# Optimization experiments

Hardware: AMD Instinct MI355X
Metric: run time of the kernel (lower is better)

## Reference

```python
import jax, jax.numpy as jnp
import numpy as np

NUM_HEADS = 16

def setup_inputs() -> dict:
    key = jax.random.key(0)
    ks = jax.random.split(key, 7)
    query_dim, kv_dim, out_dim = 1024, 768, 1024
    N, Lq, Lkv = 4, 2048, 2048
    s_q = 1.0 / np.sqrt(query_dim)
    s_kv = 1.0 / np.sqrt(kv_dim)
    return {
        "query": jax.random.normal(ks[0], (N, Lq, query_dim), dtype=jnp.float32),
        "kv": jax.random.normal(ks[1], (N, Lkv, kv_dim), dtype=jnp.float32),
        # Linear weights stored as (in_dim, out_dim) for x @ W
        "Wq": jax.random.uniform(ks[2], (query_dim, query_dim), jnp.float32, -s_q, s_q),
        "Wk": jax.random.uniform(ks[3], (kv_dim, query_dim), jnp.float32, -s_kv, s_kv),
        "Wv": jax.random.uniform(ks[4], (kv_dim, query_dim), jnp.float32, -s_kv, s_kv),
        "Wo": jax.random.uniform(ks[5], (query_dim, out_dim), jnp.float32, -s_q, s_q),
        "bo": jax.random.uniform(ks[6], (out_dim,), jnp.float32, -s_q, s_q),
    }

def reference(query, kv, Wq, Wk, Wv, Wo, bo):
    N, Lq, qd = query.shape
    Lkv = kv.shape[1]
    H = NUM_HEADS
    hd = qd // H
    scale = hd ** -0.5
    # projections -> (N, H, L, hd)
    q = (query @ Wq).reshape(N, Lq, H, hd).transpose(0, 2, 1, 3)
    k = (kv @ Wk).reshape(N, Lkv, H, hd).transpose(0, 2, 1, 3)
    v = (kv @ Wv).reshape(N, Lkv, H, hd).transpose(0, 2, 1, 3)
    # fp32 attention: (N, H, Lq, Lkv)
    attn = jnp.einsum('bhqd,bhkd->bhqk', q.astype(jnp.float32) * scale, k.astype(jnp.float32))
    attn = jax.nn.softmax(attn, axis=-1)
    out = jnp.einsum('bhqk,bhkd->bhqd', attn, v.astype(jnp.float32))
    out = out.transpose(0, 2, 1, 3).reshape(N, Lq, qd)
    return out @ Wo + bo
```

## Files before the change

kernel.cpp:

```cpp
#include <hip/hip_runtime.h>

typedef __attribute__((ext_vector_type(4))) float f32x4;
typedef __attribute__((ext_vector_type(8))) __bf16 bf16x8;
typedef __attribute__((ext_vector_type(8))) unsigned short us8;

__device__ __forceinline__ unsigned short f2bf(float f) {
    unsigned u = __builtin_bit_cast(unsigned, f);
    u += 0x7fffu + ((u >> 16) & 1u);
    return (unsigned short)(u >> 16);
}

__device__ __forceinline__ float exp2v(float x) {
    float r;
    asm("v_exp_f32 %0, %1" : "=v"(r) : "v"(x));
    return r;
}

__device__ __forceinline__ f32x4 mfma16(bf16x8 a, bf16x8 b, f32x4 c) {
    return __builtin_amdgcn_mfma_f32_16x16x32_bf16(a, b, c, 0, 0, 0);
}

__device__ __forceinline__ void gload16(const void* g, void* l) {
    __builtin_amdgcn_global_load_lds(
        (const __attribute__((address_space(1))) unsigned int*)g,
        (__attribute__((address_space(3))) unsigned int*)l, 16, 0, 0);
}

__global__ __launch_bounds__(256) void conv2_bf16(const float* __restrict__ a,
                                                  unsigned short* __restrict__ oa,
                                                  int na8,
                                                  const float* __restrict__ b,
                                                  unsigned short* __restrict__ ob,
                                                  int nb8) {
    int i = blockIdx.x * 256 + threadIdx.x;
    const float* in;
    unsigned short* out;
    if (i < na8) {
        in = a; out = oa;
    } else {
        i -= na8;
        if (i >= nb8) return;
        in = b; out = ob;
    }
    const float4* p = (const float4*)in + (size_t)i * 2;
    float4 x = p[0], y = p[1];
    us8 o;
    o[0] = f2bf(x.x); o[1] = f2bf(x.y); o[2] = f2bf(x.z); o[3] = f2bf(x.w);
    o[4] = f2bf(y.x); o[5] = f2bf(y.y); o[6] = f2bf(y.z); o[7] = f2bf(y.w);
    *((us8*)out + i) = o;
}

__global__ __launch_bounds__(256) void wtrans_all(const float* __restrict__ Wq,
                                                  const float* __restrict__ Wk,
                                                  const float* __restrict__ Wv,
                                                  const float* __restrict__ Wo,
                                                  unsigned short* __restrict__ WqT,
                                                  unsigned short* __restrict__ WkT,
                                                  unsigned short* __restrict__ WvT,
                                                  unsigned short* __restrict__ WoT,
                                                  float qscale) {
    __shared__ float t[32][33];
    int y = blockIdx.y;
    const float* in; unsigned short* out; int R; float scale = 1.0f;
    if (y < 32)      { in = Wq; out = WqT; R = 1024; scale = qscale; }
    else if (y < 56) { in = Wk; out = WkT; R = 768;  y -= 32; }
    else if (y < 80) { in = Wv; out = WvT; R = 768;  y -= 56; }
    else             { in = Wo; out = WoT; R = 1024; y -= 80; }
    int tx = threadIdx.x, ty = threadIdx.y;
    int r0 = y * 32, c0 = blockIdx.x * 32;
#pragma unroll
    for (int k = 0; k < 4; ++k)
        t[ty + k * 8][tx] = in[(size_t)(r0 + ty + k * 8) * 1024 + c0 + tx];
    __syncthreads();
#pragma unroll
    for (int k = 0; k < 4; ++k)
        out[(size_t)(c0 + ty + k * 8) * R + r0 + tx] = f2bf(t[tx][ty + k * 8] * scale);
}

template <int KD, int EPI>
__global__ __launch_bounds__(256, 4) void gemm_bf16(const unsigned short* __restrict__ A,
                                                    const unsigned short* __restrict__ B,
                                                    void* __restrict__ Cout,
                                                    const float* __restrict__ bias) {
    __shared__ __align__(16) unsigned short SL[2][8192];
    const int m0 = blockIdx.y * 128;
    const int n0 = blockIdx.x * 128;
    const int tid = threadIdx.x;
    const int w = tid >> 6, l = tid & 63;
    const int lr = l & 15, lg = l >> 4;
    const int wm = (w >> 1) * 64, wn = (w & 1) * 64;

    f32x4 acc[4][4] = {};

    int ci0 = w * 64 + l;
    int r0 = ci0 >> 2, c0 = (ci0 & 3) ^ (r0 & 3);
    int ci1 = 256 + ci0;
    int r1 = ci1 >> 2, c1 = (ci1 & 3) ^ (r1 & 3);

    const unsigned short* Ag0 = A + (size_t)(m0 + r0) * KD + c0 * 8;
    const unsigned short* Ag1 = A + (size_t)(m0 + r1) * KD + c1 * 8;
    const unsigned short* Bg0 = B + (size_t)(n0 + r0) * KD + c0 * 8;
    const unsigned short* Bg1 = B + (size_t)(n0 + r1) * KD + c1 * 8;

#define STG(buf, k0)                                                  \
    do {                                                              \
        gload16(Ag0 + (k0), &SL[buf][w * 512]);                       \
        gload16(Ag1 + (k0), &SL[buf][2048 + w * 512]);                \
        gload16(Bg0 + (k0), &SL[buf][4096 + w * 512]);                \
        gload16(Bg1 + (k0), &SL[buf][4096 + 2048 + w * 512]);         \
    } while (0)

    constexpr int NT = KD / 32;
    STG(0, 0);
    int buf = 0;
    for (int kt = 0; kt < NT; ++kt) {
        if (kt + 1 < NT) {
            STG(buf ^ 1, (kt + 1) * 32);
            asm volatile("s_waitcnt vmcnt(4)" ::: "memory");
        } else {
            asm volatile("s_waitcnt vmcnt(0)" ::: "memory");
        }
        __builtin_amdgcn_s_barrier();
        const unsigned short* Alc = &SL[buf][0];
        const unsigned short* Blc = &SL[buf][4096];
        bf16x8 af[4], bfr[4];
#pragma unroll
        for (int t = 0; t < 4; ++t) {
            int ar = wm + t * 16 + lr;
            af[t] = *(const bf16x8*)&Alc[ar * 32 + ((lg ^ (ar & 3)) * 8)];
            int br = wn + t * 16 + lr;
            bfr[t] = *(const bf16x8*)&Blc[br * 32 + ((lg ^ (br & 3)) * 8)];
        }
#pragma unroll
        for (int i = 0; i < 4; ++i)
#pragma unroll
            for (int j = 0; j < 4; ++j)
                acc[i][j] = mfma16(af[i], bfr[j], acc[i][j]);
        __builtin_amdgcn_s_barrier();
        buf ^= 1;
    }
#undef STG

#pragma unroll
    for (int i = 0; i < 4; ++i)
#pragma unroll
        for (int j = 0; j < 4; ++j)
#pragma unroll
            for (int r = 0; r < 4; ++r) {
                int m = m0 + wm + i * 16 + lg * 4 + r;
                int n = n0 + wn + j * 16 + lr;
                if (EPI == 0) {
                    int b = m >> 11, ql = m & 2047, h = n >> 6, d = n & 63;
                    ((unsigned short*)Cout)[(((size_t)(b * 16 + h) * 2048 + ql) << 6) + d] =
                        f2bf(acc[i][j][r]);
                } else {
                    ((float*)Cout)[(size_t)m * 1024 + n] = acc[i][j][r] + bias[n];
                }
            }
}

__global__ __launch_bounds__(256, 4) void gemm_kv(const unsigned short* __restrict__ A,
                                                  const unsigned short* __restrict__ Bk,
                                                  const unsigned short* __restrict__ Bv,
                                                  unsigned short* __restrict__ Ck,
                                                  unsigned short* __restrict__ Cv) {
    constexpr int KD = 768;
    __shared__ __align__(16) unsigned short SL[2][8192];
    const int isV = blockIdx.x >> 3;
    const int n0 = (blockIdx.x & 7) * 128;
    const int m0 = blockIdx.y * 128;
    const unsigned short* B = isV ? Bv : Bk;
    const int tid = threadIdx.x;
    const int w = tid >> 6, l = tid & 63;
    const int lr = l & 15, lg = l >> 4;
    const int wm = (w >> 1) * 64, wn = (w & 1) * 64;

    f32x4 acc[4][4] = {};

    int ci0 = w * 64 + l;
    int r0 = ci0 >> 2, c0 = (ci0 & 3) ^ (r0 & 3);
    int ci1 = 256 + ci0;
    int r1 = ci1 >> 2, c1 = (ci1 & 3) ^ (r1 & 3);

    const unsigned short* Ag0 = A + (size_t)(m0 + r0) * KD + c0 * 8;
    const unsigned short* Ag1 = A + (size_t)(m0 + r1) * KD + c1 * 8;
    const unsigned short* Bg0 = B + (size_t)(n0 + r0) * KD + c0 * 8;
    const unsigned short* Bg1 = B + (size_t)(n0 + r1) * KD + c1 * 8;

#define STG(buf, k0)                                                  \
    do {                                                              \
        gload16(Ag0 + (k0), &SL[buf][w * 512]);                       \
        gload16(Ag1 + (k0), &SL[buf][2048 + w * 512]);                \
        gload16(Bg0 + (k0), &SL[buf][4096 + w * 512]);                \
        gload16(Bg1 + (k0), &SL[buf][4096 + 2048 + w * 512]);         \
    } while (0)

    constexpr int NT = KD / 32;
    STG(0, 0);
    int buf = 0;
    for (int kt = 0; kt < NT; ++kt) {
        if (kt + 1 < NT) {
            STG(buf ^ 1, (kt + 1) * 32);
            asm volatile("s_waitcnt vmcnt(4)" ::: "memory");
        } else {
            asm volatile("s_waitcnt vmcnt(0)" ::: "memory");
        }
        __builtin_amdgcn_s_barrier();
        const unsigned short* Alc = &SL[buf][0];
        const unsigned short* Blc = &SL[buf][4096];
        bf16x8 af[4], bfr[4];
#pragma unroll
        for (int t = 0; t < 4; ++t) {
            int ar = wm + t * 16 + lr;
            af[t] = *(const bf16x8*)&Alc[ar * 32 + ((lg ^ (ar & 3)) * 8)];
            int br = wn + t * 16 + lr;
            bfr[t] = *(const bf16x8*)&Blc[br * 32 + ((lg ^ (br & 3)) * 8)];
        }
#pragma unroll
        for (int i = 0; i < 4; ++i)
#pragma unroll
            for (int j = 0; j < 4; ++j)
                acc[i][j] = mfma16(af[i], bfr[j], acc[i][j]);
        __builtin_amdgcn_s_barrier();
        buf ^= 1;
    }
#undef STG

    if (!isV) {
#pragma unroll
        for (int i = 0; i < 4; ++i)
#pragma unroll
            for (int j = 0; j < 4; ++j)
#pragma unroll
                for (int r = 0; r < 4; ++r) {
                    int m = m0 + wm + i * 16 + lg * 4 + r;
                    int n = n0 + wn + j * 16 + lr;
                    int b = m >> 11, ql = m & 2047, h = n >> 6, d = n & 63;
                    Ck[(((size_t)(b * 16 + h) * 2048 + ql) << 6) + d] = f2bf(acc[i][j][r]);
                }
    } else {
        const int b = m0 >> 11;
        const int mloc = m0 & 2047;
        const int h0 = n0 >> 6;
#pragma unroll
        for (int hp = 0; hp < 2; ++hp) {
            unsigned short* VTb = Cv + (size_t)(b * 16 + h0 + hp) * (64 * 2048);
#pragma unroll
            for (int dh = 0; dh < 2; ++dh) {
                __syncthreads();
                if ((w & 1) == hp) {
#pragma unroll
                    for (int jj = 0; jj < 2; ++jj) {
                        int j = dh * 2 + jj;
                        int dl = jj * 16 + lr;
#pragma unroll
                        for (int i = 0; i < 4; ++i)
#pragma unroll
                            for (int r = 0; r < 4; ++r) {
                                int kvl = wm + i * 16 + lg * 4 + r;
                                int pl = (kvl & 0x60) | (((kvl >> 2) & 3) << 3) |
                                         (((kvl >> 4) & 1) << 2) | (kvl & 3);
                                SL[0][dl * 136 + pl] = f2bf(acc[i][j][r]);
                            }
                    }
                }
                __syncthreads();
#pragma unroll
                for (int cc = 0; cc < 2; ++cc) {
                    int idx = cc * 256 + tid;
                    int row = idx >> 4, col = (idx & 15) * 8;
                    *(us8*)&VTb[(size_t)(dh * 32 + row) * 2048 + mloc + col] =
                        *(const us8*)&SL[0][row * 136 + col];
                }
            }
        }
    }
}

__global__ __launch_bounds__(256, 4) void attn_fwd(const unsigned short* __restrict__ Q,
                                                   const unsigned short* __restrict__ K,
                                                   const unsigned short* __restrict__ VT,
                                                   unsigned short* __restrict__ O) {
    __shared__ __align__(16) unsigned short Kl[2][64 * 64];
    __shared__ __align__(16) unsigned short Vl[2][64 * 64];
    const int id = blockIdx.x;
    const int sw = (id & 7) * 128 + (id >> 3);
    const int qt = sw & 15, bh = sw >> 4;
    const int tid = threadIdx.x;
    const int w = tid >> 6, l = tid & 63;
    const int lr = l & 15, lg = l >> 4;
    const size_t hbase = (size_t)bh * (2048 * 64);
    const size_t vbase = (size_t)bh * (64 * 2048);
    const int qbase = qt * 128 + w * 32;

    bf16x8 qf[2][2];
#pragma unroll
    for (int rt = 0; rt < 2; ++rt) {
        const unsigned short* qp = Q + hbase + (size_t)(qbase + rt * 16 + lr) * 64;
        qf[rt][0] = *(const bf16x8*)(qp + lg * 8);
        qf[rt][1] = *(const bf16x8*)(qp + 32 + lg * 8);
    }

    f32x4 oacc[2][4] = {};
    f32x4 lacc[2] = {};
    const f32x4 FZERO = {};

    bf16x8 ONES;
#pragma unroll
    for (int e = 0; e < 8; ++e) ONES[e] = (__bf16)1.0f;

    const int cA = tid, cB = 256 + tid;
    const int krA = cA >> 3, kcA = (cA & 7) ^ (krA & 7);
    const int krB = cB >> 3, kcB = (cB & 7) ^ (krB & 7);
    const unsigned short* Kg0 = K + hbase + (size_t)krA * 64 + kcA * 8;
    const unsigned short* Kg1 = K + hbase + (size_t)krB * 64 + kcB * 8;
    const unsigned short* Vg0 = VT + vbase + (size_t)krA * 2048 + kcA * 8;
    const unsigned short* Vg1 = VT + vbase + (size_t)krB * 2048 + kcB * 8;

#define STAGE_KV(dst, kv0)                                                    \
    do {                                                                      \
        gload16(Kg0 + (size_t)(kv0) * 64, &Kl[dst][w * 512]);                 \
        gload16(Kg1 + (size_t)(kv0) * 64, &Kl[dst][2048 + w * 512]);          \
        gload16(Vg0 + (kv0), &Vl[dst][w * 512]);                              \
        gload16(Vg1 + (kv0), &Vl[dst][2048 + w * 512]);                       \
    } while (0)

    const int koff0 = lr * 64 + ((lg ^ (lr & 7)) * 8);
    const int koff1 = lr * 64 + (((4 + lg) ^ (lr & 7)) * 8);

    STAGE_KV(0, 0);
    int cur = 0;

    for (int t = 0; t < 32; ++t) {
        if (t < 31) {
            STAGE_KV(cur ^ 1, (t + 1) * 64);
            asm volatile("s_waitcnt vmcnt(4)" ::: "memory");
        } else {
            asm volatile("s_waitcnt vmcnt(0)" ::: "memory");
        }
        __builtin_amdgcn_s_barrier();
        const unsigned short* Kc = Kl[cur];
        const unsigned short* Vc = Vl[cur];

        f32x4 s[2][4];
        __builtin_amdgcn_s_setprio(1);
#pragma unroll
        for (int nt = 0; nt < 4; ++nt) {
            bf16x8 kf0 = *(const bf16x8*)&Kc[koff0 + nt * 1024];
            bf16x8 kf1 = *(const bf16x8*)&Kc[koff1 + nt * 1024];
            s[0][nt] = mfma16(kf0, qf[0][0], FZERO);
            s[0][nt] = mfma16(kf1, qf[0][1], s[0][nt]);
            s[1][nt] = mfma16(kf0, qf[1][0], FZERO);
            s[1][nt] = mfma16(kf1, qf[1][1], s[1][nt]);
        }
        __builtin_amdgcn_s_setprio(0);

        bf16x8 pa0[2], pa1[2];
#pragma unroll
        for (int rt = 0; rt < 2; ++rt) {
#pragma unroll
            for (int nt = 0; nt < 4; ++nt)
#pragma unroll
                for (int r = 0; r < 4; ++r)
                    s[rt][nt][r] = exp2v(s[rt][nt][r]);
#pragma unroll
            for (int e = 0; e < 4; ++e) {
                pa0[rt][e] = (__bf16)s[rt][0][e];
                pa0[rt][4 + e] = (__bf16)s[rt][1][e];
                pa1[rt][e] = (__bf16)s[rt][2][e];
                pa1[rt][4 + e] = (__bf16)s[rt][3][e];
            }
        }

        __builtin_amdgcn_s_setprio(1);
        lacc[0] = mfma16(pa0[0], ONES, lacc[0]);
        lacc[0] = mfma16(pa1[0], ONES, lacc[0]);
        lacc[1] = mfma16(pa0[1], ONES, lacc[1]);
        lacc[1] = mfma16(pa1[1], ONES, lacc[1]);

#pragma unroll
        for (int nt = 0; nt < 4; ++nt) {
            bf16x8 vb0 = *(const bf16x8*)&Vc[koff0 + nt * 1024];
            bf16x8 vb1 = *(const bf16x8*)&Vc[koff1 + nt * 1024];
            oacc[0][nt] = mfma16(pa0[0], vb0, oacc[0][nt]);
            oacc[0][nt] = mfma16(pa1[0], vb1, oacc[0][nt]);
            oacc[1][nt] = mfma16(pa0[1], vb0, oacc[1][nt]);
            oacc[1][nt] = mfma16(pa1[1], vb1, oacc[1][nt]);
        }
        __builtin_amdgcn_s_setprio(0);
        __builtin_amdgcn_s_barrier();
        cur ^= 1;
    }
#undef STAGE_KV

    const int b = bh >> 4, h = bh & 15;
#pragma unroll
    for (int rt = 0; rt < 2; ++rt)
#pragma unroll
        for (int r = 0; r < 4; ++r) {
            float inv = 1.0f / lacc[rt][r];
            int q = qbase + rt * 16 + lg * 4 + r;
            size_t rowbase = ((size_t)(b * 2048 + q)) * 1024 + h * 64;
#pragma unroll
            for (int nt = 0; nt < 4; ++nt)
                O[rowbase + nt * 16 + lr] = f2bf(oacc[rt][nt][r] * inv);
        }
}

extern "C" void kernel_launch(void* const* d_in, const int* in_sizes, int n_in,
                              void* d_out, int out_size, void* d_ws, size_t ws_size,
                              hipStream_t stream) {
    (void)in_sizes; (void)n_in; (void)out_size; (void)ws_size;
    const float* query = (const float*)d_in[0];
    const float* kv    = (const float*)d_in[1];
    const float* Wq    = (const float*)d_in[2];
    const float* Wk    = (const float*)d_in[3];
    const float* Wv    = (const float*)d_in[4];
    const float* Wo    = (const float*)d_in[5];
    const float* bo    = (const float*)d_in[6];
    float* out = (float*)d_out;

    char* ws = (char*)d_ws;
    unsigned short* qbf  = (unsigned short*)(ws + 0);
    unsigned short* kvbf = (unsigned short*)(ws + 16777216);
    unsigned short* WkT  = (unsigned short*)(ws + 29360128);
    unsigned short* WvT  = (unsigned short*)(ws + 30932992);
    unsigned short* WqT  = (unsigned short*)(ws + 32505856);
    unsigned short* WoT  = (unsigned short*)(ws + 34603008);
    unsigned short* Qh   = (unsigned short*)(ws + 36700160);
    unsigned short* Kh   = (unsigned short*)(ws + 53477376);
    unsigned short* VTh  = (unsigned short*)(ws + 0);
    unsigned short* Ob   = (unsigned short*)(ws + 16777216);

    const float QSCALE = 0.18033688011112042f;

    conv2_bf16<<<7168, 256, 0, stream>>>(query, qbf, 1048576, kv, kvbf, 786432);
    wtrans_all<<<dim3(32, 112), dim3(32, 8), 0, stream>>>(Wq, Wk, Wv, Wo,
                                                          WqT, WkT, WvT, WoT, QSCALE);

    gemm_bf16<1024, 0><<<dim3(8, 64), 256, 0, stream>>>(qbf, WqT, Qh, nullptr);
    gemm_kv<<<dim3(16, 64), 256, 0, stream>>>(kvbf, WkT, WvT, Kh, VTh);
    attn_fwd<<<1024, 256, 0, stream>>>(Qh, Kh, VTh, Ob);
    gemm_bf16<1024, 1><<<dim3(8, 64), 256, 0, stream>>>(Ob, WoT, out, bo);
}
```

Measured before the change: 175.4 us.

## Merge Q/K/V projections into one launch and software-pipeline attention QK with PV

The separate Q and KV projection GEMMs become a single 1536-block launch that picks its operand by block index, with an XCD-aware block swizzle for L2 locality. The output GEMM gets the same swizzle. The attention loop is restructured so K and V tiles are staged separately and the QK^T of the next tile is issued alongside the PV of the current tile, overlapping exp work with MFMA. Attention launch bounds drop to 3 waves per SIMD to allow more registers. VTh moves to its own workspace region so it no longer aliases qbf. The cost is extra register pressure and a more complex prologue and epilogue.

```diff
diff --git a/kernel.cpp b/kernel.cpp
--- a/kernel.cpp
+++ b/kernel.cpp
@@ -77,14 +77,27 @@
         out[(size_t)(c0 + ty + k * 8) * R + r0 + tx] = f2bf(t[tx][ty + k * 8] * scale);
 }
 
-template <int KD, int EPI>
-__global__ __launch_bounds__(256, 4) void gemm_bf16(const unsigned short* __restrict__ A,
-                                                    const unsigned short* __restrict__ B,
-                                                    void* __restrict__ Cout,
-                                                    const float* __restrict__ bias) {
+__global__ __launch_bounds__(256, 4) void proj_qkv(const unsigned short* __restrict__ qbf,
+                                                   const unsigned short* __restrict__ kvbf,
+                                                   const unsigned short* __restrict__ WqT,
+                                                   const unsigned short* __restrict__ WkT,
+                                                   const unsigned short* __restrict__ WvT,
+                                                   unsigned short* __restrict__ Qh,
+                                                   unsigned short* __restrict__ Kh,
+                                                   unsigned short* __restrict__ VTh) {
     __shared__ __align__(16) unsigned short SL[2][8192];
-    const int m0 = blockIdx.y * 128;
-    const int n0 = blockIdx.x * 128;
+    const int id = blockIdx.x;
+    const int xcd = id & 7, j = id >> 3;
+    const int my = xcd * 8 + (j & 7);
+    const int rest = j >> 3;
+    const int op = rest >> 3;
+    const int nx = rest & 7;
+    const int m0 = my * 128, n0 = nx * 128;
+    const unsigned short* A = (op == 0) ? qbf : kvbf;
+    const unsigned short* B = (op == 0) ? WqT : (op == 1 ? WkT : WvT);
+    const int KD = (op == 0) ? 1024 : 768;
+    const int NT = KD >> 5;
+
     const int tid = threadIdx.x;
     const int w = tid >> 6, l = tid & 63;
     const int lr = l & 15, lg = l >> 4;
@@ -110,7 +123,6 @@
         gload16(Bg1 + (k0), &SL[buf][4096 + 2048 + w * 512]);         \
     } while (0)
 
-    constexpr int NT = KD / 32;
     STG(0, 0);
     int buf = 0;
     for (int kt = 0; kt < NT; ++kt) {
@@ -134,42 +146,75 @@
 #pragma unroll
         for (int i = 0; i < 4; ++i)
 #pragma unroll
-            for (int j = 0; j < 4; ++j)
-                acc[i][j] = mfma16(af[i], bfr[j], acc[i][j]);
+            for (int jj = 0; jj < 4; ++jj)
+                acc[i][jj] = mfma16(af[i], bfr[jj], acc[i][jj]);
         __builtin_amdgcn_s_barrier();
         buf ^= 1;
     }
 #undef STG
 
-#pragma unroll
-    for (int i = 0; i < 4; ++i)
-#pragma unroll
-        for (int j = 0; j < 4; ++j)
-#pragma unroll
-            for (int r = 0; r < 4; ++r) {
-                int m = m0 + wm + i * 16 + lg * 4 + r;
-                int n = n0 + wn + j * 16 + lr;
-                if (EPI == 0) {
+    if (op != 2) {
+        unsigned short* Cout = (op == 0) ? Qh : Kh;
+#pragma unroll
+        for (int i = 0; i < 4; ++i)
+#pragma unroll
+            for (int jj = 0; jj < 4; ++jj)
+#pragma unroll
+                for (int r = 0; r < 4; ++r) {
+                    int m = m0 + wm + i * 16 + lg * 4 + r;
+                    int n = n0 + wn + jj * 16 + lr;
                     int b = m >> 11, ql = m & 2047, h = n >> 6, d = n & 63;
-                    ((unsigned short*)Cout)[(((size_t)(b * 16 + h) * 2048 + ql) << 6) + d] =
-                        f2bf(acc[i][j][r]);
-                } else {
-                    ((float*)Cout)[(size_t)m * 1024 + n] = acc[i][j][r] + bias[n];
+                    Cout[(((size_t)(b * 16 + h) * 2048 + ql) << 6) + d] = f2bf(acc[i][jj][r]);
+                }
+    } else {
+        const int b = m0 >> 11;
+        const int mloc = m0 & 2047;
+        const int h0 = n0 >> 6;
+#pragma unroll
+        for (int hp = 0; hp < 2; ++hp) {
+            unsigned short* VTb = VTh + (size_t)(b * 16 + h0 + hp) * (64 * 2048);
+#pragma unroll
+            for (int dh = 0; dh < 2; ++dh) {
+                __syncthreads();
+                if ((w & 1) == hp) {
+#pragma unroll
+                    for (int jj = 0; jj < 2; ++jj) {
+                        int jc = dh * 2 + jj;
+                        int dl = jj * 16 + lr;
+#pragma unroll
+                        for (int i = 0; i < 4; ++i)
+#pragma unroll
+                            for (int r = 0; r < 4; ++r) {
+                                int kvl = wm + i * 16 + lg * 4 + r;
+                                int pl = (kvl & 0x60) | (((kvl >> 2) & 3) << 3) |
+                                         (((kvl >> 4) & 1) << 2) | (kvl & 3);
+                                SL[0][dl * 136 + pl] = f2bf(acc[i][jc][r]);
+                            }
+                    }
+                }
+                __syncthreads();
+#pragma unroll
+                for (int cc = 0; cc < 2; ++cc) {
+                    int idx = cc * 256 + tid;
+                    int row = idx >> 4, col = (idx & 15) * 8;
+                    *(us8*)&VTb[(size_t)(dh * 32 + row) * 2048 + mloc + col] =
+                        *(const us8*)&SL[0][row * 136 + col];
                 }
             }
-}
-
-__global__ __launch_bounds__(256, 4) void gemm_kv(const unsigned short* __restrict__ A,
-                                                  const unsigned short* __restrict__ Bk,
-                                                  const unsigned short* __restrict__ Bv,
-                                                  unsigned short* __restrict__ Ck,
-                                                  unsigned short* __restrict__ Cv) {
-    constexpr int KD = 768;
+        }
+    }
+}
+
+__global__ __launch_bounds__(256, 4) void gemm_o(const unsigned short* __restrict__ A,
+                                                 const unsigned short* __restrict__ B,
+                                                 float* __restrict__ Cout,
+                                                 const float* __restrict__ bias) {
+    constexpr int KD = 1024;
     __shared__ __align__(16) unsigned short SL[2][8192];
-    const int isV = blockIdx.x >> 3;
-    const int n0 = (blockIdx.x & 7) * 128;
-    const int m0 = blockIdx.y * 128;
-    const unsigned short* B = isV ? Bv : Bk;
+    const int id = blockIdx.x;
+    const int xcd = id & 7, j = id >> 3;
+    const int m0 = (xcd * 8 + (j & 7)) * 128;
+    const int n0 = (j >> 3) * 128;
     const int tid = threadIdx.x;
     const int w = tid >> 6, l = tid & 63;
     const int lr = l & 15, lg = l >> 4;
@@ -195,7 +240,7 @@
         gload16(Bg1 + (k0), &SL[buf][4096 + 2048 + w * 512]);         \
     } while (0)
 
-    constexpr int NT = KD / 32;
+    constexpr int NT = KD >> 5;
     STG(0, 0);
     int buf = 0;
     for (int kt = 0; kt < NT; ++kt) {
@@ -219,65 +264,26 @@
 #pragma unroll
         for (int i = 0; i < 4; ++i)
 #pragma unroll
-            for (int j = 0; j < 4; ++j)
-                acc[i][j] = mfma16(af[i], bfr[j], acc[i][j]);
+            for (int jj = 0; jj < 4; ++jj)
+                acc[i][jj] = mfma16(af[i], bfr[jj], acc[i][jj]);
         __builtin_amdgcn_s_barrier();
         buf ^= 1;
     }
 #undef STG
 
-    if (!isV) {
-#pragma unroll
-        for (int i = 0; i < 4; ++i)
-#pragma unroll
-            for (int j = 0; j < 4; ++j)
-#pragma unroll
-                for (int r = 0; r < 4; ++r) {
-                    int m = m0 + wm + i * 16 + lg * 4 + r;
-                    int n = n0 + wn + j * 16 + lr;
-                    int b = m >> 11, ql = m & 2047, h = n >> 6, d = n & 63;
-                    Ck[(((size_t)(b * 16 + h) * 2048 + ql) << 6) + d] = f2bf(acc[i][j][r]);
-                }
-    } else {
-        const int b = m0 >> 11;
-        const int mloc = m0 & 2047;
-        const int h0 = n0 >> 6;
-#pragma unroll
-        for (int hp = 0; hp < 2; ++hp) {
-            unsigned short* VTb = Cv + (size_t)(b * 16 + h0 + hp) * (64 * 2048);
-#pragma unroll
-            for (int dh = 0; dh < 2; ++dh) {
-                __syncthreads();
-                if ((w & 1) == hp) {
-#pragma unroll
-                    for (int jj = 0; jj < 2; ++jj) {
-                        int j = dh * 2 + jj;
-                        int dl = jj * 16 + lr;
-#pragma unroll
-                        for (int i = 0; i < 4; ++i)
-#pragma unroll
-                            for (int r = 0; r < 4; ++r) {
-                                int kvl = wm + i * 16 + lg * 4 + r;
-                                int pl = (kvl & 0x60) | (((kvl >> 2) & 3) << 3) |
-                                         (((kvl >> 4) & 1) << 2) | (kvl & 3);
-                                SL[0][dl * 136 + pl] = f2bf(acc[i][j][r]);
-                            }
-                    }
-                }
-                __syncthreads();
-#pragma unroll
-                for (int cc = 0; cc < 2; ++cc) {
-                    int idx = cc * 256 + tid;
-                    int row = idx >> 4, col = (idx & 15) * 8;
-                    *(us8*)&VTb[(size_t)(dh * 32 + row) * 2048 + mloc + col] =
-                        *(const us8*)&SL[0][row * 136 + col];
-                }
+#pragma unroll
+    for (int i = 0; i < 4; ++i)
+#pragma unroll
+        for (int jj = 0; jj < 4; ++jj)
+#pragma unroll
+            for (int r = 0; r < 4; ++r) {
+                int m = m0 + wm + i * 16 + lg * 4 + r;
+                int n = n0 + wn + jj * 16 + lr;
+                Cout[(size_t)m * 1024 + n] = acc[i][jj][r] + bias[n];
             }
-        }
-    }
-}
-
-__global__ __launch_bounds__(256, 4) void attn_fwd(const unsigned short* __restrict__ Q,
+}
+
+__global__ __launch_bounds__(256, 3) void attn_fwd(const unsigned short* __restrict__ Q,
                                                    const unsigned short* __restrict__ K,
                                                    const unsigned short* __restrict__ VT,
                                                    unsigned short* __restrict__ O) {
@@ -304,6 +310,8 @@
     f32x4 oacc[2][4] = {};
     f32x4 lacc[2] = {};
     const f32x4 FZERO = {};
+    f32x4 s[2][4];
+    bf16x8 pa0[2], pa1[2];
 
     bf16x8 ONES;
 #pragma unroll
@@ -317,81 +325,108 @@
     const unsigned short* Vg0 = VT + vbase + (size_t)krA * 2048 + kcA * 8;
     const unsigned short* Vg1 = VT + vbase + (size_t)krB * 2048 + kcB * 8;
 
-#define STAGE_KV(dst, kv0)                                                    \
+#define STAGE_K(dst, tkv)                                                     \
     do {                                                                      \
-        gload16(Kg0 + (size_t)(kv0) * 64, &Kl[dst][w * 512]);                 \
-        gload16(Kg1 + (size_t)(kv0) * 64, &Kl[dst][2048 + w * 512]);          \
-        gload16(Vg0 + (kv0), &Vl[dst][w * 512]);                              \
-        gload16(Vg1 + (kv0), &Vl[dst][2048 + w * 512]);                       \
+        gload16(Kg0 + (size_t)(tkv) * 4096, &Kl[dst][w * 512]);               \
+        gload16(Kg1 + (size_t)(tkv) * 4096, &Kl[dst][2048 + w * 512]);        \
+    } while (0)
+#define STAGE_V(dst, tkv)                                                     \
+    do {                                                                      \
+        gload16(Vg0 + (size_t)(tkv) * 64, &Vl[dst][w * 512]);                 \
+        gload16(Vg1 + (size_t)(tkv) * 64, &Vl[dst][2048 + w * 512]);          \
     } while (0)
 
     const int koff0 = lr * 64 + ((lg ^ (lr & 7)) * 8);
     const int koff1 = lr * 64 + (((4 + lg) ^ (lr & 7)) * 8);
 
-    STAGE_KV(0, 0);
-    int cur = 0;
-
-    for (int t = 0; t < 32; ++t) {
-        if (t < 31) {
-            STAGE_KV(cur ^ 1, (t + 1) * 64);
+#define QK_COMPUTE(Kc)                                                        \
+    do {                                                                      \
+        _Pragma("unroll")                                                     \
+        for (int nt = 0; nt < 4; ++nt) {                                      \
+            bf16x8 kf0 = *(const bf16x8*)&(Kc)[koff0 + nt * 1024];            \
+            bf16x8 kf1 = *(const bf16x8*)&(Kc)[koff1 + nt * 1024];            \
+            s[0][nt] = mfma16(kf0, qf[0][0], FZERO);                          \
+            s[0][nt] = mfma16(kf1, qf[0][1], s[0][nt]);                       \
+            s[1][nt] = mfma16(kf0, qf[1][0], FZERO);                          \
+            s[1][nt] = mfma16(kf1, qf[1][1], s[1][nt]);                       \
+        }                                                                     \
+    } while (0)
+
+#define EXP2_PACK                                                             \
+    do {                                                                      \
+        _Pragma("unroll")                                                     \
+        for (int rt = 0; rt < 2; ++rt) {                                      \
+            _Pragma("unroll")                                                 \
+            for (int nt = 0; nt < 4; ++nt)                                    \
+                _Pragma("unroll")                                             \
+                for (int r = 0; r < 4; ++r)                                   \
+                    s[rt][nt][r] = exp2v(s[rt][nt][r]);                       \
+            _Pragma("unroll")                                                 \
+            for (int e = 0; e < 4; ++e) {                                     \
+                pa0[rt][e] = (__bf16)s[rt][0][e];                             \
+                pa0[rt][4 + e] = (__bf16)s[rt][1][e];                         \
+                pa1[rt][e] = (__bf16)s[rt][2][e];                             \
+                pa1[rt][4 + e] = (__bf16)s[rt][3][e];                         \
+            }                                                                 \
+        }                                                                     \
+    } while (0)
+
+#define PV_COMPUTE(Vc)                                                        \
+    do {                                                                      \
+        lacc[0] = mfma16(pa0[0], ONES, lacc[0]);                              \
+        lacc[0] = mfma16(pa1[0], ONES, lacc[0]);                              \
+        lacc[1] = mfma16(pa0[1], ONES, lacc[1]);                              \
+        lacc[1] = mfma16(pa1[1], ONES, lacc[1]);                              \
+        _Pragma("unroll")                                                     \
+        for (int nt = 0; nt < 4; ++nt) {                                      \
+            bf16x8 vb0 = *(const bf16x8*)&(Vc)[koff0 + nt * 1024];            \
+            bf16x8 vb1 = *(const bf16x8*)&(Vc)[koff1 + nt * 1024];            \
+            oacc[0][nt] = mfma16(pa0[0], vb0, oacc[0][nt]);                   \
+            oacc[0][nt] = mfma16(pa1[0], vb1, oacc[0][nt]);                   \
+            oacc[1][nt] = mfma16(pa0[1], vb0, oacc[1][nt]);                   \
+            oacc[1][nt] = mfma16(pa1[1], vb1, oacc[1][nt]);                   \
+        }                                                                     \
+    } while (0)
+
+    STAGE_K(0, 0);
+    asm volatile("s_waitcnt vmcnt(0)" ::: "memory");
+    __builtin_amdgcn_s_barrier();
+    STAGE_K(1, 1);
+    STAGE_V(0, 0);
+    __builtin_amdgcn_s_setprio(1);
+    QK_COMPUTE(Kl[0]);
+    __builtin_amdgcn_s_setprio(0);
+    EXP2_PACK;
+    __builtin_amdgcn_s_barrier();
+
+    for (int t = 0; t < 31; ++t) {
+        if (t <= 29) STAGE_K(t & 1, t + 2);
+        STAGE_V((t + 1) & 1, t + 1);
+        if (t <= 29) {
             asm volatile("s_waitcnt vmcnt(4)" ::: "memory");
         } else {
-            asm volatile("s_waitcnt vmcnt(0)" ::: "memory");
-        }
-        __builtin_amdgcn_s_barrier();
-        const unsigned short* Kc = Kl[cur];
-        const unsigned short* Vc = Vl[cur];
-
-        f32x4 s[2][4];
+            asm volatile("s_waitcnt vmcnt(2)" ::: "memory");
+        }
+        __builtin_amdgcn_s_barrier();
         __builtin_amdgcn_s_setprio(1);
-#pragma unroll
-        for (int nt = 0; nt < 4; ++nt) {
-            bf16x8 kf0 = *(const bf16x8*)&Kc[koff0 + nt * 1024];
-            bf16x8 kf1 = *(const bf16x8*)&Kc[koff1 + nt * 1024];
-            s[0][nt] = mfma16(kf0, qf[0][0], FZERO);
-            s[0][nt] = mfma16(kf1, qf[0][1], s[0][nt]);
-            s[1][nt] = mfma16(kf0, qf[1][0], FZERO);
-            s[1][nt] = mfma16(kf1, qf[1][1], s[1][nt]);
-        }
+        QK_COMPUTE(Kl[(t + 1) & 1]);
+        PV_COMPUTE(Vl[t & 1]);
         __builtin_amdgcn_s_setprio(0);
-
-        bf16x8 pa0[2], pa1[2];
-#pragma unroll
-        for (int rt = 0; rt < 2; ++rt) {
-#pragma unroll
-            for (int nt = 0; nt < 4; ++nt)
-#pragma unroll
-                for (int r = 0; r < 4; ++r)
-                    s[rt][nt][r] = exp2v(s[rt][nt][r]);
-#pragma unroll
-            for (int e = 0; e < 4; ++e) {
-                pa0[rt][e] = (__bf16)s[rt][0][e];
-                pa0[rt][4 + e] = (__bf16)s[rt][1][e];
-                pa1[rt][e] = (__bf16)s[rt][2][e];
-                pa1[rt][4 + e] = (__bf16)s[rt][3][e];
-            }
-        }
-
-        __builtin_amdgcn_s_setprio(1);
-        lacc[0] = mfma16(pa0[0], ONES, lacc[0]);
-        lacc[0] = mfma16(pa1[0], ONES, lacc[0]);
-        lacc[1] = mfma16(pa0[1], ONES, lacc[1]);
-        lacc[1] = mfma16(pa1[1], ONES, lacc[1]);
-
-#pragma unroll
-        for (int nt = 0; nt < 4; ++nt) {
-            bf16x8 vb0 = *(const bf16x8*)&Vc[koff0 + nt * 1024];
-            bf16x8 vb1 = *(const bf16x8*)&Vc[koff1 + nt * 1024];
-            oacc[0][nt] = mfma16(pa0[0], vb0, oacc[0][nt]);
-            oacc[0][nt] = mfma16(pa1[0], vb1, oacc[0][nt]);
-            oacc[1][nt] = mfma16(pa0[1], vb0, oacc[1][nt]);
-            oacc[1][nt] = mfma16(pa1[1], vb1, oacc[1][nt]);
-        }
-        __builtin_amdgcn_s_setprio(0);
-        __builtin_amdgcn_s_barrier();
-        cur ^= 1;
-    }
-#undef STAGE_KV
+        EXP2_PACK;
+        __builtin_amdgcn_s_barrier();
+    }
+
+    asm volatile("s_waitcnt vmcnt(0)" ::: "memory");
+    __builtin_amdgcn_s_barrier();
+    __builtin_amdgcn_s_setprio(1);
+    PV_COMPUTE(Vl[1]);
+    __builtin_amdgcn_s_setprio(0);
+
+#undef STAGE_K
+#undef STAGE_V
+#undef QK_COMPUTE
+#undef EXP2_PACK
+#undef PV_COMPUTE
 
     const int b = bh >> 4, h = bh & 15;
 #pragma unroll
@@ -429,7 +464,7 @@
     unsigned short* WoT  = (unsigned short*)(ws + 34603008);
     unsigned short* Qh   = (unsigned short*)(ws + 36700160);
     unsigned short* Kh   = (unsigned short*)(ws + 53477376);
-    unsigned short* VTh  = (unsigned short*)(ws + 0);
+    unsigned short* VTh  = (unsigned short*)(ws + 70254592);
     unsigned short* Ob   = (unsigned short*)(ws + 16777216);
 
     const float QSCALE = 0.18033688011112042f;
@@ -438,8 +473,7 @@
     wtrans_all<<<dim3(32, 112), dim3(32, 8), 0, stream>>>(Wq, Wk, Wv, Wo,
                                                           WqT, WkT, WvT, WoT, QSCALE);
 
-    gemm_bf16<1024, 0><<<dim3(8, 64), 256, 0, stream>>>(qbf, WqT, Qh, nullptr);
-    gemm_kv<<<dim3(16, 64), 256, 0, stream>>>(kvbf, WkT, WvT, Kh, VTh);
+    proj_qkv<<<1536, 256, 0, stream>>>(qbf, kvbf, WqT, WkT, WvT, Qh, Kh, VTh);
     attn_fwd<<<1024, 256, 0, stream>>>(Qh, Kh, VTh, Ob);
-    gemm_bf16<1024, 1><<<dim3(8, 64), 256, 0, stream>>>(Ob, WoT, out, bo);
-}
+    gemm_o<<<512, 256, 0, stream>>>(Ob, WoT, out, bo);
+}
```

Result: no change. 175.8 us (+0.2%).

## Merge Q/K/V projections into one launch, XCD-aware tiling, larger attention q-tiles

Applied to the files above, without the earlier changes.

Combines the Q projection and the K/V projection into a single 1536-block kernel and gives it and the output GEMM an XCD-aware block-index swizzle so neighbouring M tiles share an L2. The attention kernel now handles 256 query rows per block (64 per wave) instead of 128, which halves the number of times K/V tiles are reloaded, at the cost of more registers (launch bounds lowered to 2 blocks per CU). VTh moves to its own workspace region because Q and KV are now produced concurrently and it can no longer reuse the qbf buffer.

```diff
diff --git a/kernel.cpp b/kernel.cpp
--- a/kernel.cpp
+++ b/kernel.cpp
@@ -77,14 +77,27 @@
         out[(size_t)(c0 + ty + k * 8) * R + r0 + tx] = f2bf(t[tx][ty + k * 8] * scale);
 }
 
-template <int KD, int EPI>
-__global__ __launch_bounds__(256, 4) void gemm_bf16(const unsigned short* __restrict__ A,
-                                                    const unsigned short* __restrict__ B,
-                                                    void* __restrict__ Cout,
-                                                    const float* __restrict__ bias) {
+__global__ __launch_bounds__(256, 4) void proj_qkv(const unsigned short* __restrict__ qbf,
+                                                   const unsigned short* __restrict__ kvbf,
+                                                   const unsigned short* __restrict__ WqT,
+                                                   const unsigned short* __restrict__ WkT,
+                                                   const unsigned short* __restrict__ WvT,
+                                                   unsigned short* __restrict__ Qh,
+                                                   unsigned short* __restrict__ Kh,
+                                                   unsigned short* __restrict__ VTh) {
     __shared__ __align__(16) unsigned short SL[2][8192];
-    const int m0 = blockIdx.y * 128;
-    const int n0 = blockIdx.x * 128;
+    const int id = blockIdx.x;
+    const int xcd = id & 7, j = id >> 3;
+    const int my = xcd * 8 + (j & 7);
+    const int rest = j >> 3;
+    const int op = rest >> 3;
+    const int nx = rest & 7;
+    const int m0 = my * 128, n0 = nx * 128;
+    const unsigned short* A = (op == 0) ? qbf : kvbf;
+    const unsigned short* B = (op == 0) ? WqT : (op == 1 ? WkT : WvT);
+    const int KD = (op == 0) ? 1024 : 768;
+    const int NT = KD >> 5;
+
     const int tid = threadIdx.x;
     const int w = tid >> 6, l = tid & 63;
     const int lr = l & 15, lg = l >> 4;
@@ -110,7 +123,6 @@
         gload16(Bg1 + (k0), &SL[buf][4096 + 2048 + w * 512]);         \
     } while (0)
 
-    constexpr int NT = KD / 32;
     STG(0, 0);
     int buf = 0;
     for (int kt = 0; kt < NT; ++kt) {
@@ -134,42 +146,75 @@
 #pragma unroll
         for (int i = 0; i < 4; ++i)
 #pragma unroll
-            for (int j = 0; j < 4; ++j)
-                acc[i][j] = mfma16(af[i], bfr[j], acc[i][j]);
+            for (int jj = 0; jj < 4; ++jj)
+                acc[i][jj] = mfma16(af[i], bfr[jj], acc[i][jj]);
         __builtin_amdgcn_s_barrier();
         buf ^= 1;
     }
 #undef STG
 
-#pragma unroll
-    for (int i = 0; i < 4; ++i)
-#pragma unroll
-        for (int j = 0; j < 4; ++j)
-#pragma unroll
-            for (int r = 0; r < 4; ++r) {
-                int m = m0 + wm + i * 16 + lg * 4 + r;
-                int n = n0 + wn + j * 16 + lr;
-                if (EPI == 0) {
+    if (op != 2) {
+        unsigned short* Cout = (op == 0) ? Qh : Kh;
+#pragma unroll
+        for (int i = 0; i < 4; ++i)
+#pragma unroll
+            for (int jj = 0; jj < 4; ++jj)
+#pragma unroll
+                for (int r = 0; r < 4; ++r) {
+                    int m = m0 + wm + i * 16 + lg * 4 + r;
+                    int n = n0 + wn + jj * 16 + lr;
                     int b = m >> 11, ql = m & 2047, h = n >> 6, d = n & 63;
-                    ((unsigned short*)Cout)[(((size_t)(b * 16 + h) * 2048 + ql) << 6) + d] =
-                        f2bf(acc[i][j][r]);
-                } else {
-                    ((float*)Cout)[(size_t)m * 1024 + n] = acc[i][j][r] + bias[n];
+                    Cout[(((size_t)(b * 16 + h) * 2048 + ql) << 6) + d] = f2bf(acc[i][jj][r]);
+                }
+    } else {
+        const int b = m0 >> 11;
+        const int mloc = m0 & 2047;
+        const int h0 = n0 >> 6;
+#pragma unroll
+        for (int hp = 0; hp < 2; ++hp) {
+            unsigned short* VTb = VTh + (size_t)(b * 16 + h0 + hp) * (64 * 2048);
+#pragma unroll
+            for (int dh = 0; dh < 2; ++dh) {
+                __syncthreads();
+                if ((w & 1) == hp) {
+#pragma unroll
+                    for (int jj = 0; jj < 2; ++jj) {
+                        int jc = dh * 2 + jj;
+                        int dl = jj * 16 + lr;
+#pragma unroll
+                        for (int i = 0; i < 4; ++i)
+#pragma unroll
+                            for (int r = 0; r < 4; ++r) {
+                                int kvl = wm + i * 16 + lg * 4 + r;
+                                int pl = (kvl & 0x60) | (((kvl >> 2) & 3) << 3) |
+                                         (((kvl >> 4) & 1) << 2) | (kvl & 3);
+                                SL[0][dl * 136 + pl] = f2bf(acc[i][jc][r]);
+                            }
+                    }
+                }
+                __syncthreads();
+#pragma unroll
+                for (int cc = 0; cc < 2; ++cc) {
+                    int idx = cc * 256 + tid;
+                    int row = idx >> 4, col = (idx & 15) * 8;
+                    *(us8*)&VTb[(size_t)(dh * 32 + row) * 2048 + mloc + col] =
+                        *(const us8*)&SL[0][row * 136 + col];
                 }
             }
-}
-
-__global__ __launch_bounds__(256, 4) void gemm_kv(const unsigned short* __restrict__ A,
-                                                  const unsigned short* __restrict__ Bk,
-                                                  const unsigned short* __restrict__ Bv,
-                                                  unsigned short* __restrict__ Ck,
-                                                  unsigned short* __restrict__ Cv) {
-    constexpr int KD = 768;
+        }
+    }
+}
+
+__global__ __launch_bounds__(256, 4) void gemm_o(const unsigned short* __restrict__ A,
+                                                 const unsigned short* __restrict__ B,
+                                                 float* __restrict__ Cout,
+                                                 const float* __restrict__ bias) {
+    constexpr int KD = 1024;
     __shared__ __align__(16) unsigned short SL[2][8192];
-    const int isV = blockIdx.x >> 3;
-    const int n0 = (blockIdx.x & 7) * 128;
-    const int m0 = blockIdx.y * 128;
-    const unsigned short* B = isV ? Bv : Bk;
+    const int id = blockIdx.x;
+    const int xcd = id & 7, j = id >> 3;
+    const int m0 = (xcd * 8 + (j & 7)) * 128;
+    const int n0 = (j >> 3) * 128;
     const int tid = threadIdx.x;
     const int w = tid >> 6, l = tid & 63;
     const int lr = l & 15, lg = l >> 4;
@@ -195,7 +240,7 @@
         gload16(Bg1 + (k0), &SL[buf][4096 + 2048 + w * 512]);         \
     } while (0)
 
-    constexpr int NT = KD / 32;
+    constexpr int NT = KD >> 5;
     STG(0, 0);
     int buf = 0;
     for (int kt = 0; kt < NT; ++kt) {
@@ -219,90 +264,51 @@
 #pragma unroll
         for (int i = 0; i < 4; ++i)
 #pragma unroll
-            for (int j = 0; j < 4; ++j)
-                acc[i][j] = mfma16(af[i], bfr[j], acc[i][j]);
+            for (int jj = 0; jj < 4; ++jj)
+                acc[i][jj] = mfma16(af[i], bfr[jj], acc[i][jj]);
         __builtin_amdgcn_s_barrier();
         buf ^= 1;
     }
 #undef STG
 
-    if (!isV) {
-#pragma unroll
-        for (int i = 0; i < 4; ++i)
-#pragma unroll
-            for (int j = 0; j < 4; ++j)
-#pragma unroll
-                for (int r = 0; r < 4; ++r) {
-                    int m = m0 + wm + i * 16 + lg * 4 + r;
-                    int n = n0 + wn + j * 16 + lr;
-                    int b = m >> 11, ql = m & 2047, h = n >> 6, d = n & 63;
-                    Ck[(((size_t)(b * 16 + h) * 2048 + ql) << 6) + d] = f2bf(acc[i][j][r]);
-                }
-    } else {
-        const int b = m0 >> 11;
-        const int mloc = m0 & 2047;
-        const int h0 = n0 >> 6;
-#pragma unroll
-        for (int hp = 0; hp < 2; ++hp) {
-            unsigned short* VTb = Cv + (size_t)(b * 16 + h0 + hp) * (64 * 2048);
-#pragma unroll
-            for (int dh = 0; dh < 2; ++dh) {
-                __syncthreads();
-                if ((w & 1) == hp) {
-#pragma unroll
-                    for (int jj = 0; jj < 2; ++jj) {
-                        int j = dh * 2 + jj;
-                        int dl = jj * 16 + lr;
-#pragma unroll
-                        for (int i = 0; i < 4; ++i)
-#pragma unroll
-                            for (int r = 0; r < 4; ++r) {
-                                int kvl = wm + i * 16 + lg * 4 + r;
-                                int pl = (kvl & 0x60) | (((kvl >> 2) & 3) << 3) |
-                                         (((kvl >> 4) & 1) << 2) | (kvl & 3);
-                                SL[0][dl * 136 + pl] = f2bf(acc[i][j][r]);
-                            }
-                    }
-                }
-                __syncthreads();
-#pragma unroll
-                for (int cc = 0; cc < 2; ++cc) {
-                    int idx = cc * 256 + tid;
-                    int row = idx >> 4, col = (idx & 15) * 8;
-                    *(us8*)&VTb[(size_t)(dh * 32 + row) * 2048 + mloc + col] =
-                        *(const us8*)&SL[0][row * 136 + col];
-                }
+#pragma unroll
+    for (int i = 0; i < 4; ++i)
+#pragma unroll
+        for (int jj = 0; jj < 4; ++jj)
+#pragma unroll
+            for (int r = 0; r < 4; ++r) {
+                int m = m0 + wm + i * 16 + lg * 4 + r;
+                int n = n0 + wn + jj * 16 + lr;
+                Cout[(size_t)m * 1024 + n] = acc[i][jj][r] + bias[n];
             }
-        }
-    }
-}
-
-__global__ __launch_bounds__(256, 4) void attn_fwd(const unsigned short* __restrict__ Q,
+}
+
+__global__ __launch_bounds__(256, 2) void attn_fwd(const unsigned short* __restrict__ Q,
                                                    const unsigned short* __restrict__ K,
                                                    const unsigned short* __restrict__ VT,
                                                    unsigned short* __restrict__ O) {
     __shared__ __align__(16) unsigned short Kl[2][64 * 64];
     __shared__ __align__(16) unsigned short Vl[2][64 * 64];
     const int id = blockIdx.x;
-    const int sw = (id & 7) * 128 + (id >> 3);
-    const int qt = sw & 15, bh = sw >> 4;
+    const int sw = (id & 7) * 64 + (id >> 3);
+    const int qt = sw & 7, bh = sw >> 3;
     const int tid = threadIdx.x;
     const int w = tid >> 6, l = tid & 63;
     const int lr = l & 15, lg = l >> 4;
     const size_t hbase = (size_t)bh * (2048 * 64);
     const size_t vbase = (size_t)bh * (64 * 2048);
-    const int qbase = qt * 128 + w * 32;
-
-    bf16x8 qf[2][2];
-#pragma unroll
-    for (int rt = 0; rt < 2; ++rt) {
+    const int qbase = qt * 256 + w * 64;
+
+    bf16x8 qf[4][2];
+#pragma unroll
+    for (int rt = 0; rt < 4; ++rt) {
         const unsigned short* qp = Q + hbase + (size_t)(qbase + rt * 16 + lr) * 64;
         qf[rt][0] = *(const bf16x8*)(qp + lg * 8);
         qf[rt][1] = *(const bf16x8*)(qp + 32 + lg * 8);
     }
 
-    f32x4 oacc[2][4] = {};
-    f32x4 lacc[2] = {};
+    f32x4 oacc[4][4] = {};
+    f32x4 lacc[4] = {};
     const f32x4 FZERO = {};
 
     bf16x8 ONES;
@@ -342,22 +348,23 @@
         const unsigned short* Kc = Kl[cur];
         const unsigned short* Vc = Vl[cur];
 
-        f32x4 s[2][4];
+        f32x4 s[4][4];
         __builtin_amdgcn_s_setprio(1);
 #pragma unroll
         for (int nt = 0; nt < 4; ++nt) {
             bf16x8 kf0 = *(const bf16x8*)&Kc[koff0 + nt * 1024];
             bf16x8 kf1 = *(const bf16x8*)&Kc[koff1 + nt * 1024];
-            s[0][nt] = mfma16(kf0, qf[0][0], FZERO);
-            s[0][nt] = mfma16(kf1, qf[0][1], s[0][nt]);
-            s[1][nt] = mfma16(kf0, qf[1][0], FZERO);
-            s[1][nt] = mfma16(kf1, qf[1][1], s[1][nt]);
+#pragma unroll
+            for (int rt = 0; rt < 4; ++rt) {
+                s[rt][nt] = mfma16(kf0, qf[rt][0], FZERO);
+                s[rt][nt] = mfma16(kf1, qf[rt][1], s[rt][nt]);
+            }
         }
         __builtin_amdgcn_s_setprio(0);
 
-        bf16x8 pa0[2], pa1[2];
-#pragma unroll
-        for (int rt = 0; rt < 2; ++rt) {
+        bf16x8 pa0[4], pa1[4];
+#pragma unroll
+        for (int rt = 0; rt < 4; ++rt) {
 #pragma unroll
             for (int nt = 0; nt < 4; ++nt)
 #pragma unroll
@@ -373,19 +380,20 @@
         }
 
         __builtin_amdgcn_s_setprio(1);
-        lacc[0] = mfma16(pa0[0], ONES, lacc[0]);
-        lacc[0] = mfma16(pa1[0], ONES, lacc[0]);
-        lacc[1] = mfma16(pa0[1], ONES, lacc[1]);
-        lacc[1] = mfma16(pa1[1], ONES, lacc[1]);
-
+#pragma unroll
+        for (int rt = 0; rt < 4; ++rt) {
+            lacc[rt] = mfma16(pa0[rt], ONES, lacc[rt]);
+            lacc[rt] = mfma16(pa1[rt], ONES, lacc[rt]);
+        }
 #pragma unroll
         for (int nt = 0; nt < 4; ++nt) {
             bf16x8 vb0 = *(const bf16x8*)&Vc[koff0 + nt * 1024];
             bf16x8 vb1 = *(const bf16x8*)&Vc[koff1 + nt * 1024];
-            oacc[0][nt] = mfma16(pa0[0], vb0, oacc[0][nt]);
-            oacc[0][nt] = mfma16(pa1[0], vb1, oacc[0][nt]);
-            oacc[1][nt] = mfma16(pa0[1], vb0, oacc[1][nt]);
-            oacc[1][nt] = mfma16(pa1[1], vb1, oacc[1][nt]);
+#pragma unroll
+            for (int rt = 0; rt < 4; ++rt) {
+                oacc[rt][nt] = mfma16(pa0[rt], vb0, oacc[rt][nt]);
+                oacc[rt][nt] = mfma16(pa1[rt], vb1, oacc[rt][nt]);
+            }
         }
         __builtin_amdgcn_s_setprio(0);
         __builtin_amdgcn_s_barrier();
@@ -395,7 +403,7 @@
 
     const int b = bh >> 4, h = bh & 15;
 #pragma unroll
-    for (int rt = 0; rt < 2; ++rt)
+    for (int rt = 0; rt < 4; ++rt)
 #pragma unroll
         for (int r = 0; r < 4; ++r) {
             float inv = 1.0f / lacc[rt][r];
@@ -429,7 +437,7 @@
     unsigned short* WoT  = (unsigned short*)(ws + 34603008);
     unsigned short* Qh   = (unsigned short*)(ws + 36700160);
     unsigned short* Kh   = (unsigned short*)(ws + 53477376);
-    unsigned short* VTh  = (unsigned short*)(ws + 0);
+    unsigned short* VTh  = (unsigned short*)(ws + 70254592);
     unsigned short* Ob   = (unsigned short*)(ws + 16777216);
 
     const float QSCALE = 0.18033688011112042f;
@@ -438,8 +446,7 @@
     wtrans_all<<<dim3(32, 112), dim3(32, 8), 0, stream>>>(Wq, Wk, Wv, Wo,
                                                           WqT, WkT, WvT, WoT, QSCALE);
 
-    gemm_bf16<1024, 0><<<dim3(8, 64), 256, 0, stream>>>(qbf, WqT, Qh, nullptr);
-    gemm_kv<<<dim3(16, 64), 256, 0, stream>>>(kvbf, WkT, WvT, Kh, VTh);
-    attn_fwd<<<1024, 256, 0, stream>>>(Qh, Kh, VTh, Ob);
-    gemm_bf16<1024, 1><<<dim3(8, 64), 256, 0, stream>>>(Ob, WoT, out, bo);
-}
+    proj_qkv<<<1536, 256, 0, stream>>>(qbf, kvbf, WqT, WkT, WvT, Qh, Kh, VTh);
+    attn_fwd<<<512, 256, 0, stream>>>(Qh, Kh, VTh, Ob);
+    gemm_o<<<512, 256, 0, stream>>>(Ob, WoT, out, bo);
+}
```

After: 161.8 us. 1.08x faster.
